# Performance work log

Hardware: AMD Instinct MI355X
Metric: run time of the kernel (lower is better)

## Reference

```python
import jax, jax.numpy as jnp
import numpy as np
from jax.ops import segment_sum

N, E, F, H, G, T = 50000, 800000, 128, 256, 512, 4


def setup_inputs() -> dict:
    key = jax.random.key(0)
    ks = jax.random.split(key, 12)
    x = jax.random.normal(ks[0], (N, F), jnp.float32)
    edge_index = jax.random.randint(ks[1], (2, E), 0, N)
    batch = jnp.sort(jax.random.randint(ks[2], (N,), 0, G))
    num_atoms = jax.random.normal(ks[3], (G, 1), jnp.float32)
    def lin(k, fan_in, fan_out):
        s = 1.0 / np.sqrt(fan_in)
        return jax.random.uniform(k, (fan_in, fan_out), jnp.float32, -s, s)
    W1 = lin(ks[4], F, H); b1 = jnp.zeros((H,), jnp.float32)
    W2 = lin(ks[5], H, H); b2 = jnp.zeros((H,), jnp.float32)
    W3 = lin(ks[6], H + 1, 32); b3 = jnp.zeros((32,), jnp.float32)
    W4 = lin(ks[7], 32, T); b4 = jnp.zeros((T,), jnp.float32)
    return {"x": x, "edge_index": edge_index, "batch": batch, "num_atoms": num_atoms,
            "W1": W1, "b1": b1, "W2": W2, "b2": b2, "W3": W3, "b3": b3, "W4": W4, "b4": b4}


def _gcn_norm(edge_index, num_nodes):
    # PyG GCNConv default: add self-loops, symmetric D^-1/2 A D^-1/2 normalization
    loop = jnp.arange(num_nodes, dtype=edge_index.dtype)
    src = jnp.concatenate([edge_index[0], loop])
    dst = jnp.concatenate([edge_index[1], loop])
    deg = segment_sum(jnp.ones_like(dst, jnp.float32), dst, num_segments=num_nodes)
    dinv = jnp.where(deg > 0, jax.lax.rsqrt(jnp.maximum(deg, 1e-12)), 0.0)
    norm = dinv[src] * dinv[dst]  # [E+N]
    return src, dst, norm


def _gcn_conv(x, W, b, src, dst, norm, num_nodes):
    h = x @ W  # [N, out]
    agg = segment_sum(h[src] * norm[:, None], dst, num_segments=num_nodes)
    return agg + b


def reference(x, edge_index, batch, num_atoms, W1, b1, W2, b2, W3, b3, W4, b4):
    n = x.shape[0]
    src, dst, norm = _gcn_norm(edge_index, n)
    h = jax.nn.relu(_gcn_conv(x, W1, b1, src, dst, norm, n))   # dropout = identity (eval)
    h = jax.nn.relu(_gcn_conv(h, W2, b2, src, dst, norm, n))
    # global mean pool over graphs
    sums = segment_sum(h, batch, num_segments=G)               # [G, H]
    cnt = segment_sum(jnp.ones((n,), jnp.float32), batch, num_segments=G)
    pooled = sums / jnp.maximum(cnt, 1.0)[:, None]
    z = jnp.concatenate([pooled, num_atoms], axis=1)           # [G, H+1]
    z = jax.nn.relu(z @ W3 + b3)
    return z @ W4 + b4                                         # [G, T]
```

## Files before the change

### kernel.cpp

```cpp
#include <hip/hip_runtime.h>
#include <hip/hip_bf16.h>


#define NN 50000
#define EE 800000
#define FDIM 128
#define HDIM 256
#define GG 512
#define SCAN_NB ((NN + 255) / 256)

typedef __attribute__((ext_vector_type(8))) short short8;
typedef __attribute__((ext_vector_type(4))) float floatx4;

__device__ __forceinline__ unsigned short f2bf(float f) {
    unsigned u = __float_as_uint(f);
    return (unsigned short)((u + 0x7FFF + ((u >> 16) & 1)) >> 16);
}
__device__ __forceinline__ float bflo(unsigned v) { return __uint_as_float(v << 16); }
__device__ __forceinline__ float bfhi(unsigned v) { return __uint_as_float(v & 0xFFFF0000u); }


__global__ __launch_bounds__(256) void zero_bufs(int* __restrict__ deg, float* __restrict__ pool) {
    int i = blockIdx.x * 256 + threadIdx.x;
    int stride = gridDim.x * 256;
    for (int k = i; k < NN; k += stride) deg[k] = 0;
    for (int k = i; k < GG * HDIM; k += stride) pool[k] = 0.f;
}

__global__ void hist_kernel(const int* __restrict__ dst, int* __restrict__ deg, int e) {
    int i = blockIdx.x * blockDim.x + threadIdx.x;
    int stride = gridDim.x * blockDim.x;
    for (; i < e; i += stride) atomicAdd(&deg[dst[i]], 1);
}

__global__ __launch_bounds__(256) void scan_part(const int* __restrict__ deg,
                                                 int* __restrict__ row_off,
                                                 int* __restrict__ blk_sums,
                                                 float* __restrict__ dinv, int n) {
    __shared__ int s[256];
    int tid = threadIdx.x;
    int i = blockIdx.x * 256 + tid;
    int v = (i < n) ? deg[i] : 0;
    if (i < n) dinv[i] = rsqrtf((float)v + 1.0f);
    s[tid] = v;
    __syncthreads();
    #pragma unroll
    for (int off = 1; off < 256; off <<= 1) {
        int t = (tid >= off) ? s[tid - off] : 0;
        __syncthreads();
        s[tid] += t;
        __syncthreads();
    }
    if (i < n) row_off[i] = s[tid] - v;
    if (tid == 255) blk_sums[blockIdx.x] = s[255];
}

__global__ __launch_bounds__(256) void scan_sums(int* __restrict__ blk_sums, int nb) {
    __shared__ int s[256];
    int tid = threadIdx.x;
    int v = (tid < nb) ? blk_sums[tid] : 0;
    s[tid] = v;
    __syncthreads();
    #pragma unroll
    for (int off = 1; off < 256; off <<= 1) {
        int t = (tid >= off) ? s[tid - off] : 0;
        __syncthreads();
        s[tid] += t;
        __syncthreads();
    }
    if (tid < nb) blk_sums[tid] = s[tid] - v;
}

__global__ __launch_bounds__(256) void scan_add(int* __restrict__ row_off,
                                                const int* __restrict__ blk_sums,
                                                int* __restrict__ fill, int n, int e) {
    int i = blockIdx.x * 256 + threadIdx.x;
    if (i < n) {
        row_off[i] += blk_sums[blockIdx.x];
        fill[i] = 0;
    }
    if (i == 0) row_off[n] = e;
}

__global__ void scatter_kernel(const int* __restrict__ src, const int* __restrict__ dst,
                               const int* __restrict__ row_off, int* __restrict__ fill,
                               const float* __restrict__ dinv,
                               int2* __restrict__ csr, int e) {
    int i = blockIdx.x * blockDim.x + threadIdx.x;
    int stride = gridDim.x * blockDim.x;
    for (; i < e; i += stride) {
        int s = src[i], d = dst[i];
        int pos = row_off[d] + atomicAdd(&fill[d], 1);
        csr[pos] = make_int2(s, __float_as_int(dinv[s] * dinv[d]));
    }
}

#define XCHUNKS (NN * FDIM / 4)
__global__ __launch_bounds__(256) void cast_all(const float* __restrict__ x,
                                                unsigned short* __restrict__ x_bf,
                                                const float* __restrict__ W1,
                                                unsigned short* __restrict__ W1t,
                                                const float* __restrict__ W2,
                                                unsigned short* __restrict__ W2t) {
    int idx = blockIdx.x * 256 + threadIdx.x;
    if (idx < XCHUNKS) {
        int i = idx * 4;
        float4 v = *(const float4*)&x[i];
        ushort4 o;
        o.x = f2bf(v.x); o.y = f2bf(v.y); o.z = f2bf(v.z); o.w = f2bf(v.w);
        *(ushort4*)&x_bf[i] = o;
        return;
    }
    int r = idx - XCHUNKS;
    if (r < FDIM * HDIM) {
        int nn = r / FDIM, k = r - nn * FDIM;
        W1t[r] = f2bf(W1[(size_t)k * HDIM + nn]);
        return;
    }
    r -= FDIM * HDIM;
    if (r < HDIM * HDIM) {
        int nn = r / HDIM, k = r - nn * HDIM;
        W2t[r] = f2bf(W2[(size_t)k * HDIM + nn]);
    }
}


#define FMA8(v, wgt) do { unsigned _u; \
    _u = (unsigned)(v).x; acc0 = fmaf(bflo(_u), (wgt), acc0); acc1 = fmaf(bfhi(_u), (wgt), acc1); \
    _u = (unsigned)(v).y; acc2 = fmaf(bflo(_u), (wgt), acc2); acc3 = fmaf(bfhi(_u), (wgt), acc3); \
    _u = (unsigned)(v).z; acc4 = fmaf(bflo(_u), (wgt), acc4); acc5 = fmaf(bfhi(_u), (wgt), acc5); \
    _u = (unsigned)(v).w; acc6 = fmaf(bflo(_u), (wgt), acc6); acc7 = fmaf(bfhi(_u), (wgt), acc7); } while (0)

__global__ __launch_bounds__(256) void gcn_agg256_bf16(const unsigned short* __restrict__ in,
                                                       const int* __restrict__ row_off,
                                                       const int2* __restrict__ csr,
                                                       const float* __restrict__ dinv,
                                                       unsigned short* __restrict__ out, int n) {
    int wave = threadIdx.x >> 6;
    int lane = threadIdx.x & 63;
    int node = blockIdx.x * 4 + wave;
    if (node >= n) return;
    int sub = lane >> 5;
    int fl  = lane & 31;
    float di = dinv[node];
    float w0 = (sub == 0) ? di * di : 0.f;

    float acc0, acc1, acc2, acc3, acc4, acc5, acc6, acc7;
    {
        int4 sv = *(const int4*)&in[(size_t)node * 256 + fl * 8];
        unsigned _u;
        _u = (unsigned)sv.x; acc0 = bflo(_u) * w0; acc1 = bfhi(_u) * w0;
        _u = (unsigned)sv.y; acc2 = bflo(_u) * w0; acc3 = bfhi(_u) * w0;
        _u = (unsigned)sv.z; acc4 = bflo(_u) * w0; acc5 = bfhi(_u) * w0;
        _u = (unsigned)sv.w; acc6 = bflo(_u) * w0; acc7 = bfhi(_u) * w0;
    }

    int beg = __builtin_amdgcn_readfirstlane(row_off[node]);
    int end = __builtin_amdgcn_readfirstlane(row_off[node + 1]);
    int cnt = end - beg;
    if (cnt > 0) {
        int nIter = (cnt + 7) >> 3;
        int base = beg;
        int last = end - 1;
        int i0 = base + 0 + sub, i1 = base + 2 + sub, i2 = base + 4 + sub, i3 = base + 6 + sub;
        int2 c0 = csr[i0 < end ? i0 : last];
        int2 c1 = csr[i1 < end ? i1 : last];
        int2 c2 = csr[i2 < end ? i2 : last];
        int2 c3 = csr[i3 < end ? i3 : last];
        for (int it = 0; it < nIter; ++it) {
            int4 g0 = *(const int4*)&in[(size_t)c0.x * 256 + fl * 8];
            int4 g1 = *(const int4*)&in[(size_t)c1.x * 256 + fl * 8];
            int4 g2 = *(const int4*)&in[(size_t)c2.x * 256 + fl * 8];
            int4 g3 = *(const int4*)&in[(size_t)c3.x * 256 + fl * 8];
            float we0 = (base + 0 + sub < end) ? __int_as_float(c0.y) : 0.f;
            float we1 = (base + 2 + sub < end) ? __int_as_float(c1.y) : 0.f;
            float we2 = (base + 4 + sub < end) ? __int_as_float(c2.y) : 0.f;
            float we3 = (base + 6 + sub < end) ? __int_as_float(c3.y) : 0.f;
            int nb = base + 8;
            int j0 = nb + 0 + sub, j1 = nb + 2 + sub, j2 = nb + 4 + sub, j3 = nb + 6 + sub;
            int2 n0 = csr[j0 < end ? j0 : last];
            int2 n1 = csr[j1 < end ? j1 : last];
            int2 n2 = csr[j2 < end ? j2 : last];
            int2 n3 = csr[j3 < end ? j3 : last];
            FMA8(g0, we0); FMA8(g1, we1); FMA8(g2, we2); FMA8(g3, we3);
            c0 = n0; c1 = n1; c2 = n2; c3 = n3; base = nb;
        }
    }
    acc0 += __shfl_xor(acc0, 32); acc1 += __shfl_xor(acc1, 32);
    acc2 += __shfl_xor(acc2, 32); acc3 += __shfl_xor(acc3, 32);
    acc4 += __shfl_xor(acc4, 32); acc5 += __shfl_xor(acc5, 32);
    acc6 += __shfl_xor(acc6, 32); acc7 += __shfl_xor(acc7, 32);
    if (sub == 0) {
        int4 o;
        o.x = (int)((unsigned)f2bf(acc0) | ((unsigned)f2bf(acc1) << 16));
        o.y = (int)((unsigned)f2bf(acc2) | ((unsigned)f2bf(acc3) << 16));
        o.z = (int)((unsigned)f2bf(acc4) | ((unsigned)f2bf(acc5) << 16));
        o.w = (int)((unsigned)f2bf(acc6) | ((unsigned)f2bf(acc7) << 16));
        *(int4*)&out[(size_t)node * 256 + fl * 8] = o;
    }
}

__global__ __launch_bounds__(256) void gcn_agg128_bf16(const unsigned short* __restrict__ in,
                                                       const int* __restrict__ row_off,
                                                       const int2* __restrict__ csr,
                                                       const float* __restrict__ dinv,
                                                       unsigned short* __restrict__ out, int n) {
    int wave = threadIdx.x >> 6;
    int lane = threadIdx.x & 63;
    int node = blockIdx.x * 4 + wave;
    if (node >= n) return;
    int sub = lane >> 4;
    int fl  = lane & 15;
    float di = dinv[node];
    float w0 = (sub == 0) ? di * di : 0.f;

    float acc0, acc1, acc2, acc3, acc4, acc5, acc6, acc7;
    {
        int4 sv = *(const int4*)&in[(size_t)node * 128 + fl * 8];
        unsigned _u;
        _u = (unsigned)sv.x; acc0 = bflo(_u) * w0; acc1 = bfhi(_u) * w0;
        _u = (unsigned)sv.y; acc2 = bflo(_u) * w0; acc3 = bfhi(_u) * w0;
        _u = (unsigned)sv.z; acc4 = bflo(_u) * w0; acc5 = bfhi(_u) * w0;
        _u = (unsigned)sv.w; acc6 = bflo(_u) * w0; acc7 = bfhi(_u) * w0;
    }

    int beg = __builtin_amdgcn_readfirstlane(row_off[node]);
    int end = __builtin_amdgcn_readfirstlane(row_off[node + 1]);
    int cnt = end - beg;
    if (cnt > 0) {
        int nIter = (cnt + 7) >> 3;
        int base = beg;
        int last = end - 1;
        int i0 = base + sub, i1 = base + 4 + sub;
        int2 c0 = csr[i0 < end ? i0 : last];
        int2 c1 = csr[i1 < end ? i1 : last];
        for (int it = 0; it < nIter; ++it) {
            int4 g0 = *(const int4*)&in[(size_t)c0.x * 128 + fl * 8];
            int4 g1 = *(const int4*)&in[(size_t)c1.x * 128 + fl * 8];
            float we0 = (base + sub < end) ? __int_as_float(c0.y) : 0.f;
            float we1 = (base + 4 + sub < end) ? __int_as_float(c1.y) : 0.f;
            int nb = base + 8;
            int j0 = nb + sub, j1 = nb + 4 + sub;
            int2 n0 = csr[j0 < end ? j0 : last];
            int2 n1 = csr[j1 < end ? j1 : last];
            FMA8(g0, we0); FMA8(g1, we1);
            c0 = n0; c1 = n1; base = nb;
        }
    }
    acc0 += __shfl_xor(acc0, 16); acc1 += __shfl_xor(acc1, 16);
    acc2 += __shfl_xor(acc2, 16); acc3 += __shfl_xor(acc3, 16);
    acc4 += __shfl_xor(acc4, 16); acc5 += __shfl_xor(acc5, 16);
    acc6 += __shfl_xor(acc6, 16); acc7 += __shfl_xor(acc7, 16);
    acc0 += __shfl_xor(acc0, 32); acc1 += __shfl_xor(acc1, 32);
    acc2 += __shfl_xor(acc2, 32); acc3 += __shfl_xor(acc3, 32);
    acc4 += __shfl_xor(acc4, 32); acc5 += __shfl_xor(acc5, 32);
    acc6 += __shfl_xor(acc6, 32); acc7 += __shfl_xor(acc7, 32);
    if (sub == 0) {
        int4 o;
        o.x = (int)((unsigned)f2bf(acc0) | ((unsigned)f2bf(acc1) << 16));
        o.y = (int)((unsigned)f2bf(acc2) | ((unsigned)f2bf(acc3) << 16));
        o.z = (int)((unsigned)f2bf(acc4) | ((unsigned)f2bf(acc5) << 16));
        o.w = (int)((unsigned)f2bf(acc6) | ((unsigned)f2bf(acc7) << 16));
        *(int4*)&out[(size_t)node * 128 + fl * 8] = o;
    }
}


__global__ __launch_bounds__(512, 2) void gemm1_mfma_bias_relu(
        const unsigned short* __restrict__ A,
        const unsigned short* __restrict__ Bt,
        const float* __restrict__ bias,
        unsigned short* __restrict__ C, int M) {
    constexpr int K = FDIM, Nc = HDIM, LDT = 40;
    __shared__ unsigned short As[128 * LDT];
    __shared__ unsigned short Bs[256 * LDT];
    int tid = threadIdx.x;
    int lane = tid & 63, wave = tid >> 6;
    int wm = (wave >> 2) * 64, wn = (wave & 3) * 64;
    int bm = blockIdx.x * 128;
    int l15 = lane & 15, quad = lane >> 4;

    floatx4 zero = {0.f, 0.f, 0.f, 0.f};
    floatx4 acc[4][4];
    #pragma unroll
    for (int s = 0; s < 4; ++s)
        #pragma unroll
        for (int t = 0; t < 4; ++t) acc[s][t] = zero;

    for (int k0 = 0; k0 < K; k0 += 32) {
        {
            int row = tid >> 2, q = tid & 3;
            int4 va = {0, 0, 0, 0};
            int gr = bm + row;
            if (gr < M) va = *(const int4*)&A[(size_t)gr * K + k0 + q * 8];
            *(int4*)&As[row * LDT + q * 8] = va;
        }
        #pragma unroll
        for (int c = tid; c < 1024; c += 512) {
            int row = c >> 2, q = c & 3;
            int4 vb = *(const int4*)&Bt[(size_t)row * K + k0 + q * 8];
            *(int4*)&Bs[row * LDT + q * 8] = vb;
        }
        __syncthreads();
        short8 af[4], bf[4];
        #pragma unroll
        for (int s = 0; s < 4; ++s)
            af[s] = *(const short8*)&As[(wm + s * 16 + l15) * LDT + quad * 8];
        #pragma unroll
        for (int t = 0; t < 4; ++t)
            bf[t] = *(const short8*)&Bs[(wn + t * 16 + l15) * LDT + quad * 8];
        #pragma unroll
        for (int s = 0; s < 4; ++s)
            #pragma unroll
            for (int t = 0; t < 4; ++t)
                acc[s][t] = __builtin_amdgcn_mfma_f32_16x16x32_bf16(af[s], bf[t], acc[s][t], 0, 0, 0);
        __syncthreads();
    }
    #pragma unroll
    for (int s = 0; s < 4; ++s) {
        int row0 = bm + wm + s * 16 + quad * 4;
        #pragma unroll
        for (int t = 0; t < 4; ++t) {
            int col = wn + t * 16 + l15;
            float bb = bias[col];
            #pragma unroll
            for (int r = 0; r < 4; ++r) {
                int row = row0 + r;
                if (row < M)
                    C[(size_t)row * Nc + col] = f2bf(fmaxf(acc[s][t][r] + bb, 0.f));
            }
        }
    }
}

__global__ __launch_bounds__(512, 2) void gemm2_pool(
        const unsigned short* __restrict__ A,
        const unsigned short* __restrict__ Bt,
        const float* __restrict__ bias,
        const int* __restrict__ batch,
        float* __restrict__ pool, int M) {
    constexpr int K = HDIM, Nc = HDIM, LDT = 40;
    __shared__ unsigned short As[128 * LDT];
    __shared__ unsigned short Bs[256 * LDT];
    int tid = threadIdx.x;
    int lane = tid & 63, wave = tid >> 6;
    int wm = (wave >> 2) * 64, wn = (wave & 3) * 64;
    int bm = blockIdx.x * 128;
    int l15 = lane & 15, quad = lane >> 4;

    floatx4 zero = {0.f, 0.f, 0.f, 0.f};
    floatx4 acc[4][4];
    #pragma unroll
    for (int s = 0; s < 4; ++s)
        #pragma unroll
        for (int t = 0; t < 4; ++t) acc[s][t] = zero;

    for (int k0 = 0; k0 < K; k0 += 32) {
        {
            int row = tid >> 2, q = tid & 3;
            int4 va = {0, 0, 0, 0};
            int gr = bm + row;
            if (gr < M) va = *(const int4*)&A[(size_t)gr * K + k0 + q * 8];
            *(int4*)&As[row * LDT + q * 8] = va;
        }
        #pragma unroll
        for (int c = tid; c < 1024; c += 512) {
            int row = c >> 2, q = c & 3;
            int4 vb = *(const int4*)&Bt[(size_t)row * K + k0 + q * 8];
            *(int4*)&Bs[row * LDT + q * 8] = vb;
        }
        __syncthreads();
        short8 af[4], bf[4];
        #pragma unroll
        for (int s = 0; s < 4; ++s)
            af[s] = *(const short8*)&As[(wm + s * 16 + l15) * LDT + quad * 8];
        #pragma unroll
        for (int t = 0; t < 4; ++t)
            bf[t] = *(const short8*)&Bs[(wn + t * 16 + l15) * LDT + quad * 8];
        #pragma unroll
        for (int s = 0; s < 4; ++s)
            #pragma unroll
            for (int t = 0; t < 4; ++t)
                acc[s][t] = __builtin_amdgcn_mfma_f32_16x16x32_bf16(af[s], bf[t], acc[s][t], 0, 0, 0);
        __syncthreads();
    }
    #pragma unroll
    for (int s = 0; s < 4; ++s) {
        int row0 = bm + wm + s * 16 + quad * 4;
        if (row0 >= M) continue;
        bool full = (row0 + 3 < M);
        int gA = batch[row0];
        int gB = full ? batch[row0 + 3] : gA;
        bool same = full && (gA == gB);
        #pragma unroll
        for (int t = 0; t < 4; ++t) {
            int col = wn + t * 16 + l15;
            float bb = bias[col];
            if (same) {
                float v = fmaxf(acc[s][t][0] + bb, 0.f) + fmaxf(acc[s][t][1] + bb, 0.f)
                        + fmaxf(acc[s][t][2] + bb, 0.f) + fmaxf(acc[s][t][3] + bb, 0.f);
                atomicAdd(&pool[(size_t)gA * Nc + col], v);
            } else {
                #pragma unroll
                for (int r = 0; r < 4; ++r) {
                    int row = row0 + r;
                    if (row < M) {
                        float v = fmaxf(acc[s][t][r] + bb, 0.f);
                        atomicAdd(&pool[(size_t)batch[row] * Nc + col], v);
                    }
                }
            }
        }
    }
}


__device__ __forceinline__ int lower_bound_i(const int* __restrict__ a, int n, int v) {
    int lo = 0, hi = n;
    while (lo < hi) {
        int mid = (lo + hi) >> 1;
        if (a[mid] < v) lo = mid + 1; else hi = mid;
    }
    return lo;
}

__global__ __launch_bounds__(256) void head_kernel(const float* __restrict__ pool,
                                                   const int* __restrict__ batch,
                                                   const float* __restrict__ num_atoms,
                                                   const float* __restrict__ W3, const float* __restrict__ b3,
                                                   const float* __restrict__ W4, const float* __restrict__ b4,
                                                   float* __restrict__ out, int n) {
    int g = blockIdx.x;
    int tid = threadIdx.x;
    __shared__ int s_lo, s_hi;
    if (tid == 0) {
        s_lo = lower_bound_i(batch, n, g);
        s_hi = lower_bound_i(batch, n, g + 1);
    }
    __syncthreads();
    float cnt = (float)(s_hi - s_lo);

    __shared__ float zin[HDIM + 1];
    __shared__ float z[32];
    zin[tid] = pool[(size_t)g * HDIM + tid] / fmaxf(cnt, 1.0f);
    if (tid == 0) zin[HDIM] = num_atoms[g];
    __syncthreads();
    if (tid < 32) {
        float a = b3[tid];
        for (int k = 0; k < HDIM + 1; ++k) a = fmaf(zin[k], W3[k * 32 + tid], a);
        z[tid] = fmaxf(a, 0.f);
    }
    __syncthreads();
    if (tid < 4) {
        float a = b4[tid];
        #pragma unroll
        for (int k = 0; k < 32; ++k) a = fmaf(z[k], W4[k * 4 + tid], a);
        out[g * 4 + tid] = a;
    }
}


extern "C" void kernel_launch(void* const* d_in, const int* in_sizes, int n_in,
                              void* d_out, int out_size, void* d_ws, size_t ws_size,
                              hipStream_t stream) {
    const float* x         = (const float*)d_in[0];
    const int*   edge_idx  = (const int*)d_in[1];
    const int*   batch     = (const int*)d_in[2];
    const float* num_atoms = (const float*)d_in[3];
    const float* W1 = (const float*)d_in[4];
    const float* b1 = (const float*)d_in[5];
    const float* W2 = (const float*)d_in[6];
    const float* b2 = (const float*)d_in[7];
    const float* W3 = (const float*)d_in[8];
    const float* b3 = (const float*)d_in[9];
    const float* W4 = (const float*)d_in[10];
    const float* b4 = (const float*)d_in[11];
    float* out = (float*)d_out;

    const int n = NN, e = EE;
    const int* e_src = edge_idx;
    const int* e_dst = edge_idx + e;

    char* ws = (char*)d_ws;
    size_t off = 0;
    auto carve = [&](size_t bytes) -> void* {
        void* p = ws + off;
        off = (off + bytes + 255) & ~(size_t)255;
        return p;
    };
    int*   deg_i    = (int*)carve((size_t)n * 4);
    int*   row_off  = (int*)carve((size_t)(n + 1) * 4);
    int*   fill     = (int*)carve((size_t)n * 4);
    int*   blk_sums = (int*)carve((size_t)256 * 4);
    float* dinv     = (float*)carve((size_t)n * 4);
    unsigned short* W1t = (unsigned short*)carve((size_t)FDIM * HDIM * 2);
    unsigned short* W2t = (unsigned short*)carve((size_t)HDIM * HDIM * 2);
    int2*  csr      = (int2*)carve((size_t)e * 8);
    unsigned short* P = (unsigned short*)carve((size_t)n * HDIM * 2);
    unsigned short* Q = (unsigned short*)carve((size_t)n * HDIM * 2);
    float* pool     = (float*)carve((size_t)GG * HDIM * 4);
    unsigned short* x_bf = P;
    unsigned short* a0b  = P + (size_t)n * FDIM;
    unsigned short* a1b  = P;
    unsigned short* h1b  = Q;
    (void)ws_size; (void)n_in; (void)in_sizes; (void)out_size;

    zero_bufs<<<256, 256, 0, stream>>>(deg_i, pool);
    hist_kernel<<<1024, 256, 0, stream>>>(e_dst, deg_i, e);
    scan_part<<<SCAN_NB, 256, 0, stream>>>(deg_i, row_off, blk_sums, dinv, n);
    scan_sums<<<1, 256, 0, stream>>>(blk_sums, SCAN_NB);
    scan_add<<<SCAN_NB, 256, 0, stream>>>(row_off, blk_sums, fill, n, e);
    scatter_kernel<<<1024, 256, 0, stream>>>(e_src, e_dst, row_off, fill, dinv, csr, e);

    cast_all<<<(XCHUNKS + FDIM * HDIM + HDIM * HDIM + 255) / 256, 256, 0, stream>>>(
        x, x_bf, W1, W1t, W2, W2t);

    int gemm_grid = (n + 127) / 128;
    gcn_agg128_bf16<<<(n + 3) / 4, 256, 0, stream>>>(x_bf, row_off, csr, dinv, a0b, n);
    gemm1_mfma_bias_relu<<<gemm_grid, 512, 0, stream>>>(a0b, W1t, b1, h1b, n);
    gcn_agg256_bf16<<<(n + 3) / 4, 256, 0, stream>>>(h1b, row_off, csr, dinv, a1b, n);
    gemm2_pool<<<gemm_grid, 512, 0, stream>>>(a1b, W2t, b2, batch, pool, n);
    head_kernel<<<GG, 256, 0, stream>>>(pool, batch, num_atoms, W3, b3, W4, b4, out, n);
}
```

Baseline: 350.2 us.

## Fuse GCN neighbor aggregation into MFMA GEMM via shared-memory tile

Merges each aggregation kernel with the following GEMM. A block aggregates 32 nodes into an LDS tile, then runs MFMA against the weight matrix read straight from global memory. This drops the intermediate aggregated-activation buffers and two kernel launches. In exchange, GEMM tiles become smaller (32 rows), B fragments are re-read from global/L2 by every block, and each wave handles 8 nodes serially, which may reduce latency hiding in the gather.

```diff
diff --git a/kernel.cpp b/kernel.cpp
--- a/kernel.cpp
+++ b/kernel.cpp
@@ -131,194 +131,105 @@
     _u = (unsigned)(v).z; acc4 = fmaf(bflo(_u), (wgt), acc4); acc5 = fmaf(bfhi(_u), (wgt), acc5); \
     _u = (unsigned)(v).w; acc6 = fmaf(bflo(_u), (wgt), acc6); acc7 = fmaf(bfhi(_u), (wgt), acc7); } while (0)
 
-__global__ __launch_bounds__(256) void gcn_agg256_bf16(const unsigned short* __restrict__ in,
-                                                       const int* __restrict__ row_off,
-                                                       const int2* __restrict__ csr,
-                                                       const float* __restrict__ dinv,
-                                                       unsigned short* __restrict__ out, int n) {
-    int wave = threadIdx.x >> 6;
-    int lane = threadIdx.x & 63;
-    int node = blockIdx.x * 4 + wave;
-    if (node >= n) return;
-    int sub = lane >> 5;
-    int fl  = lane & 31;
-    float di = dinv[node];
-    float w0 = (sub == 0) ? di * di : 0.f;
-
-    float acc0, acc1, acc2, acc3, acc4, acc5, acc6, acc7;
-    {
-        int4 sv = *(const int4*)&in[(size_t)node * 256 + fl * 8];
-        unsigned _u;
-        _u = (unsigned)sv.x; acc0 = bflo(_u) * w0; acc1 = bfhi(_u) * w0;
-        _u = (unsigned)sv.y; acc2 = bflo(_u) * w0; acc3 = bfhi(_u) * w0;
-        _u = (unsigned)sv.z; acc4 = bflo(_u) * w0; acc5 = bfhi(_u) * w0;
-        _u = (unsigned)sv.w; acc6 = bflo(_u) * w0; acc7 = bfhi(_u) * w0;
-    }
-
-    int beg = __builtin_amdgcn_readfirstlane(row_off[node]);
-    int end = __builtin_amdgcn_readfirstlane(row_off[node + 1]);
-    int cnt = end - beg;
-    if (cnt > 0) {
-        int nIter = (cnt + 7) >> 3;
-        int base = beg;
-        int last = end - 1;
-        int i0 = base + 0 + sub, i1 = base + 2 + sub, i2 = base + 4 + sub, i3 = base + 6 + sub;
-        int2 c0 = csr[i0 < end ? i0 : last];
-        int2 c1 = csr[i1 < end ? i1 : last];
-        int2 c2 = csr[i2 < end ? i2 : last];
-        int2 c3 = csr[i3 < end ? i3 : last];
-        for (int it = 0; it < nIter; ++it) {
-            int4 g0 = *(const int4*)&in[(size_t)c0.x * 256 + fl * 8];
-            int4 g1 = *(const int4*)&in[(size_t)c1.x * 256 + fl * 8];
-            int4 g2 = *(const int4*)&in[(size_t)c2.x * 256 + fl * 8];
-            int4 g3 = *(const int4*)&in[(size_t)c3.x * 256 + fl * 8];
-            float we0 = (base + 0 + sub < end) ? __int_as_float(c0.y) : 0.f;
-            float we1 = (base + 2 + sub < end) ? __int_as_float(c1.y) : 0.f;
-            float we2 = (base + 4 + sub < end) ? __int_as_float(c2.y) : 0.f;
-            float we3 = (base + 6 + sub < end) ? __int_as_float(c3.y) : 0.f;
-            int nb = base + 8;
-            int j0 = nb + 0 + sub, j1 = nb + 2 + sub, j2 = nb + 4 + sub, j3 = nb + 6 + sub;
-            int2 n0 = csr[j0 < end ? j0 : last];
-            int2 n1 = csr[j1 < end ? j1 : last];
-            int2 n2 = csr[j2 < end ? j2 : last];
-            int2 n3 = csr[j3 < end ? j3 : last];
-            FMA8(g0, we0); FMA8(g1, we1); FMA8(g2, we2); FMA8(g3, we3);
-            c0 = n0; c1 = n1; c2 = n2; c3 = n3; base = nb;
-        }
-    }
-    acc0 += __shfl_xor(acc0, 32); acc1 += __shfl_xor(acc1, 32);
-    acc2 += __shfl_xor(acc2, 32); acc3 += __shfl_xor(acc3, 32);
-    acc4 += __shfl_xor(acc4, 32); acc5 += __shfl_xor(acc5, 32);
-    acc6 += __shfl_xor(acc6, 32); acc7 += __shfl_xor(acc7, 32);
-    if (sub == 0) {
-        int4 o;
-        o.x = (int)((unsigned)f2bf(acc0) | ((unsigned)f2bf(acc1) << 16));
-        o.y = (int)((unsigned)f2bf(acc2) | ((unsigned)f2bf(acc3) << 16));
-        o.z = (int)((unsigned)f2bf(acc4) | ((unsigned)f2bf(acc5) << 16));
-        o.w = (int)((unsigned)f2bf(acc6) | ((unsigned)f2bf(acc7) << 16));
-        *(int4*)&out[(size_t)node * 256 + fl * 8] = o;
-    }
-}
-
-__global__ __launch_bounds__(256) void gcn_agg128_bf16(const unsigned short* __restrict__ in,
-                                                       const int* __restrict__ row_off,
-                                                       const int2* __restrict__ csr,
-                                                       const float* __restrict__ dinv,
-                                                       unsigned short* __restrict__ out, int n) {
-    int wave = threadIdx.x >> 6;
-    int lane = threadIdx.x & 63;
-    int node = blockIdx.x * 4 + wave;
-    if (node >= n) return;
-    int sub = lane >> 4;
-    int fl  = lane & 15;
-    float di = dinv[node];
-    float w0 = (sub == 0) ? di * di : 0.f;
-
-    float acc0, acc1, acc2, acc3, acc4, acc5, acc6, acc7;
-    {
-        int4 sv = *(const int4*)&in[(size_t)node * 128 + fl * 8];
-        unsigned _u;
-        _u = (unsigned)sv.x; acc0 = bflo(_u) * w0; acc1 = bfhi(_u) * w0;
-        _u = (unsigned)sv.y; acc2 = bflo(_u) * w0; acc3 = bfhi(_u) * w0;
-        _u = (unsigned)sv.z; acc4 = bflo(_u) * w0; acc5 = bfhi(_u) * w0;
-        _u = (unsigned)sv.w; acc6 = bflo(_u) * w0; acc7 = bfhi(_u) * w0;
-    }
-
-    int beg = __builtin_amdgcn_readfirstlane(row_off[node]);
-    int end = __builtin_amdgcn_readfirstlane(row_off[node + 1]);
-    int cnt = end - beg;
-    if (cnt > 0) {
-        int nIter = (cnt + 7) >> 3;
-        int base = beg;
-        int last = end - 1;
-        int i0 = base + sub, i1 = base + 4 + sub;
-        int2 c0 = csr[i0 < end ? i0 : last];
-        int2 c1 = csr[i1 < end ? i1 : last];
-        for (int it = 0; it < nIter; ++it) {
-            int4 g0 = *(const int4*)&in[(size_t)c0.x * 128 + fl * 8];
-            int4 g1 = *(const int4*)&in[(size_t)c1.x * 128 + fl * 8];
-            float we0 = (base + sub < end) ? __int_as_float(c0.y) : 0.f;
-            float we1 = (base + 4 + sub < end) ? __int_as_float(c1.y) : 0.f;
-            int nb = base + 8;
-            int j0 = nb + sub, j1 = nb + 4 + sub;
-            int2 n0 = csr[j0 < end ? j0 : last];
-            int2 n1 = csr[j1 < end ? j1 : last];
-            FMA8(g0, we0); FMA8(g1, we1);
-            c0 = n0; c1 = n1; base = nb;
-        }
-    }
-    acc0 += __shfl_xor(acc0, 16); acc1 += __shfl_xor(acc1, 16);
-    acc2 += __shfl_xor(acc2, 16); acc3 += __shfl_xor(acc3, 16);
-    acc4 += __shfl_xor(acc4, 16); acc5 += __shfl_xor(acc5, 16);
-    acc6 += __shfl_xor(acc6, 16); acc7 += __shfl_xor(acc7, 16);
-    acc0 += __shfl_xor(acc0, 32); acc1 += __shfl_xor(acc1, 32);
-    acc2 += __shfl_xor(acc2, 32); acc3 += __shfl_xor(acc3, 32);
-    acc4 += __shfl_xor(acc4, 32); acc5 += __shfl_xor(acc5, 32);
-    acc6 += __shfl_xor(acc6, 32); acc7 += __shfl_xor(acc7, 32);
-    if (sub == 0) {
-        int4 o;
-        o.x = (int)((unsigned)f2bf(acc0) | ((unsigned)f2bf(acc1) << 16));
-        o.y = (int)((unsigned)f2bf(acc2) | ((unsigned)f2bf(acc3) << 16));
-        o.z = (int)((unsigned)f2bf(acc4) | ((unsigned)f2bf(acc5) << 16));
-        o.w = (int)((unsigned)f2bf(acc6) | ((unsigned)f2bf(acc7) << 16));
-        *(int4*)&out[(size_t)node * 128 + fl * 8] = o;
-    }
-}
-
-
-__global__ __launch_bounds__(512, 2) void gemm1_mfma_bias_relu(
-        const unsigned short* __restrict__ A,
-        const unsigned short* __restrict__ Bt,
-        const float* __restrict__ bias,
-        unsigned short* __restrict__ C, int M) {
-    constexpr int K = FDIM, Nc = HDIM, LDT = 40;
-    __shared__ unsigned short As[128 * LDT];
-    __shared__ unsigned short Bs[256 * LDT];
+__global__ __launch_bounds__(256) void agg_gemm1(const unsigned short* __restrict__ in,
+                                                 const int* __restrict__ row_off,
+                                                 const int2* __restrict__ csr,
+                                                 const float* __restrict__ dinv,
+                                                 const unsigned short* __restrict__ Bt,
+                                                 const float* __restrict__ bias,
+                                                 unsigned short* __restrict__ C, int M) {
+    constexpr int K = FDIM, Nc = HDIM, LDT = 136;
+    __shared__ unsigned short As[32 * LDT];
     int tid = threadIdx.x;
     int lane = tid & 63, wave = tid >> 6;
-    int wm = (wave >> 2) * 64, wn = (wave & 3) * 64;
-    int bm = blockIdx.x * 128;
+    int bm = blockIdx.x * 32;
+
+    {
+        int sub = lane >> 4;
+        int fl  = lane & 15;
+        for (int r8 = 0; r8 < 8; ++r8) {
+            int nodeRow = wave * 8 + r8;
+            int node = bm + nodeRow;
+            if (node >= M) break;
+            float di = dinv[node];
+            float w0 = (sub == 0) ? di * di : 0.f;
+            float acc0, acc1, acc2, acc3, acc4, acc5, acc6, acc7;
+            {
+                int4 sv = *(const int4*)&in[(size_t)node * 128 + fl * 8];
+                unsigned _u;
+                _u = (unsigned)sv.x; acc0 = bflo(_u) * w0; acc1 = bfhi(_u) * w0;
+                _u = (unsigned)sv.y; acc2 = bflo(_u) * w0; acc3 = bfhi(_u) * w0;
+                _u = (unsigned)sv.z; acc4 = bflo(_u) * w0; acc5 = bfhi(_u) * w0;
+                _u = (unsigned)sv.w; acc6 = bflo(_u) * w0; acc7 = bfhi(_u) * w0;
+            }
+            int beg = __builtin_amdgcn_readfirstlane(row_off[node]);
+            int end = __builtin_amdgcn_readfirstlane(row_off[node + 1]);
+            if (end > beg) {
+                int last = end - 1;
+                int base = beg;
+                int i0 = base + sub, i1 = base + 4 + sub;
+                int2 c0 = csr[i0 < end ? i0 : last];
+                int2 c1 = csr[i1 < end ? i1 : last];
+                int nIter = (end - beg + 7) >> 3;
+                for (int it = 0; it < nIter; ++it) {
+                    int4 g0 = *(const int4*)&in[(size_t)c0.x * 128 + fl * 8];
+                    int4 g1 = *(const int4*)&in[(size_t)c1.x * 128 + fl * 8];
+                    float we0 = (base + sub < end) ? __int_as_float(c0.y) : 0.f;
+                    float we1 = (base + 4 + sub < end) ? __int_as_float(c1.y) : 0.f;
+                    int nb = base + 8;
+                    int j0 = nb + sub, j1 = nb + 4 + sub;
+                    int2 n0 = csr[j0 < end ? j0 : last];
+                    int2 n1 = csr[j1 < end ? j1 : last];
+                    FMA8(g0, we0); FMA8(g1, we1);
+                    c0 = n0; c1 = n1; base = nb;
+                }
+            }
+            acc0 += __shfl_xor(acc0, 16); acc1 += __shfl_xor(acc1, 16);
+            acc2 += __shfl_xor(acc2, 16); acc3 += __shfl_xor(acc3, 16);
+            acc4 += __shfl_xor(acc4, 16); acc5 += __shfl_xor(acc5, 16);
+            acc6 += __shfl_xor(acc6, 16); acc7 += __shfl_xor(acc7, 16);
+            acc0 += __shfl_xor(acc0, 32); acc1 += __shfl_xor(acc1, 32);
+            acc2 += __shfl_xor(acc2, 32); acc3 += __shfl_xor(acc3, 32);
+            acc4 += __shfl_xor(acc4, 32); acc5 += __shfl_xor(acc5, 32);
+            acc6 += __shfl_xor(acc6, 32); acc7 += __shfl_xor(acc7, 32);
+            if (sub == 0) {
+                int4 o;
+                o.x = (int)((unsigned)f2bf(acc0) | ((unsigned)f2bf(acc1) << 16));
+                o.y = (int)((unsigned)f2bf(acc2) | ((unsigned)f2bf(acc3) << 16));
+                o.z = (int)((unsigned)f2bf(acc4) | ((unsigned)f2bf(acc5) << 16));
+                o.w = (int)((unsigned)f2bf(acc6) | ((unsigned)f2bf(acc7) << 16));
+                *(int4*)&As[nodeRow * LDT + fl * 8] = o;
+            }
+        }
+    }
+    __syncthreads();
+
     int l15 = lane & 15, quad = lane >> 4;
-
+    int wn = wave * 64;
     floatx4 zero = {0.f, 0.f, 0.f, 0.f};
-    floatx4 acc[4][4];
-    #pragma unroll
-    for (int s = 0; s < 4; ++s)
+    floatx4 acc[2][4];
+    #pragma unroll
+    for (int s = 0; s < 2; ++s)
         #pragma unroll
         for (int t = 0; t < 4; ++t) acc[s][t] = zero;
-
+    #pragma unroll
     for (int k0 = 0; k0 < K; k0 += 32) {
-        {
-            int row = tid >> 2, q = tid & 3;
-            int4 va = {0, 0, 0, 0};
-            int gr = bm + row;
-            if (gr < M) va = *(const int4*)&A[(size_t)gr * K + k0 + q * 8];
-            *(int4*)&As[row * LDT + q * 8] = va;
-        }
-        #pragma unroll
-        for (int c = tid; c < 1024; c += 512) {
-            int row = c >> 2, q = c & 3;
-            int4 vb = *(const int4*)&Bt[(size_t)row * K + k0 + q * 8];
-            *(int4*)&Bs[row * LDT + q * 8] = vb;
-        }
-        __syncthreads();
-        short8 af[4], bf[4];
-        #pragma unroll
-        for (int s = 0; s < 4; ++s)
-            af[s] = *(const short8*)&As[(wm + s * 16 + l15) * LDT + quad * 8];
+        short8 af[2], bf[4];
+        #pragma unroll
+        for (int s = 0; s < 2; ++s)
+            af[s] = *(const short8*)&As[(s * 16 + l15) * LDT + k0 + quad * 8];
         #pragma unroll
         for (int t = 0; t < 4; ++t)
-            bf[t] = *(const short8*)&Bs[(wn + t * 16 + l15) * LDT + quad * 8];
-        #pragma unroll
-        for (int s = 0; s < 4; ++s)
+            bf[t] = *(const short8*)&Bt[(size_t)(wn + t * 16 + l15) * K + k0 + quad * 8];
+        #pragma unroll
+        for (int s = 0; s < 2; ++s)
             #pragma unroll
             for (int t = 0; t < 4; ++t)
                 acc[s][t] = __builtin_amdgcn_mfma_f32_16x16x32_bf16(af[s], bf[t], acc[s][t], 0, 0, 0);
-        __syncthreads();
-    }
-    #pragma unroll
-    for (int s = 0; s < 4; ++s) {
-        int row0 = bm + wm + s * 16 + quad * 4;
+    }
+    #pragma unroll
+    for (int s = 0; s < 2; ++s) {
+        int row0 = bm + s * 16 + quad * 4;
         #pragma unroll
         for (int t = 0; t < 4; ++t) {
             int col = wn + t * 16 + l15;
@@ -333,60 +244,112 @@
     }
 }
 
-__global__ __launch_bounds__(512, 2) void gemm2_pool(
-        const unsigned short* __restrict__ A,
-        const unsigned short* __restrict__ Bt,
-        const float* __restrict__ bias,
-        const int* __restrict__ batch,
-        float* __restrict__ pool, int M) {
-    constexpr int K = HDIM, Nc = HDIM, LDT = 40;
-    __shared__ unsigned short As[128 * LDT];
-    __shared__ unsigned short Bs[256 * LDT];
+__global__ __launch_bounds__(256) void agg_gemm2_pool(const unsigned short* __restrict__ in,
+                                                      const int* __restrict__ row_off,
+                                                      const int2* __restrict__ csr,
+                                                      const float* __restrict__ dinv,
+                                                      const unsigned short* __restrict__ Bt,
+                                                      const float* __restrict__ bias,
+                                                      const int* __restrict__ batch,
+                                                      float* __restrict__ pool, int M) {
+    constexpr int K = HDIM, Nc = HDIM, LDT = 264;
+    __shared__ unsigned short As[32 * LDT];
     int tid = threadIdx.x;
     int lane = tid & 63, wave = tid >> 6;
-    int wm = (wave >> 2) * 64, wn = (wave & 3) * 64;
-    int bm = blockIdx.x * 128;
+    int bm = blockIdx.x * 32;
+
+    {
+        int sub = lane >> 5;
+        int fl  = lane & 31;
+        for (int r8 = 0; r8 < 8; ++r8) {
+            int nodeRow = wave * 8 + r8;
+            int node = bm + nodeRow;
+            if (node >= M) break;
+            float di = dinv[node];
+            float w0 = (sub == 0) ? di * di : 0.f;
+            float acc0, acc1, acc2, acc3, acc4, acc5, acc6, acc7;
+            {
+                int4 sv = *(const int4*)&in[(size_t)node * 256 + fl * 8];
+                unsigned _u;
+                _u = (unsigned)sv.x; acc0 = bflo(_u) * w0; acc1 = bfhi(_u) * w0;
+                _u = (unsigned)sv.y; acc2 = bflo(_u) * w0; acc3 = bfhi(_u) * w0;
+                _u = (unsigned)sv.z; acc4 = bflo(_u) * w0; acc5 = bfhi(_u) * w0;
+                _u = (unsigned)sv.w; acc6 = bflo(_u) * w0; acc7 = bfhi(_u) * w0;
+            }
+            int beg = __builtin_amdgcn_readfirstlane(row_off[node]);
+            int end = __builtin_amdgcn_readfirstlane(row_off[node + 1]);
+            if (end > beg) {
+                int last = end - 1;
+                int base = beg;
+                int i0 = base + 0 + sub, i1 = base + 2 + sub;
+                int i2 = base + 4 + sub, i3 = base + 6 + sub;
+                int2 c0 = csr[i0 < end ? i0 : last];
+                int2 c1 = csr[i1 < end ? i1 : last];
+                int2 c2 = csr[i2 < end ? i2 : last];
+                int2 c3 = csr[i3 < end ? i3 : last];
+                int nIter = (end - beg + 7) >> 3;
+                for (int it = 0; it < nIter; ++it) {
+                    int4 g0 = *(const int4*)&in[(size_t)c0.x * 256 + fl * 8];
+                    int4 g1 = *(const int4*)&in[(size_t)c1.x * 256 + fl * 8];
+                    int4 g2 = *(const int4*)&in[(size_t)c2.x * 256 + fl * 8];
+                    int4 g3 = *(const int4*)&in[(size_t)c3.x * 256 + fl * 8];
+                    float we0 = (base + 0 + sub < end) ? __int_as_float(c0.y) : 0.f;
+                    float we1 = (base + 2 + sub < end) ? __int_as_float(c1.y) : 0.f;
+                    float we2 = (base + 4 + sub < end) ? __int_as_float(c2.y) : 0.f;
+                    float we3 = (base + 6 + sub < end) ? __int_as_float(c3.y) : 0.f;
+                    int nb = base + 8;
+                    int j0 = nb + 0 + sub, j1 = nb + 2 + sub;
+                    int j2 = nb + 4 + sub, j3 = nb + 6 + sub;
+                    int2 n0 = csr[j0 < end ? j0 : last];
+                    int2 n1 = csr[j1 < end ? j1 : last];
+                    int2 n2 = csr[j2 < end ? j2 : last];
+                    int2 n3 = csr[j3 < end ? j3 : last];
+                    FMA8(g0, we0); FMA8(g1, we1); FMA8(g2, we2); FMA8(g3, we3);
+                    c0 = n0; c1 = n1; c2 = n2; c3 = n3; base = nb;
+                }
+            }
+            acc0 += __shfl_xor(acc0, 32); acc1 += __shfl_xor(acc1, 32);
+            acc2 += __shfl_xor(acc2, 32); acc3 += __shfl_xor(acc3, 32);
+            acc4 += __shfl_xor(acc4, 32); acc5 += __shfl_xor(acc5, 32);
+            acc6 += __shfl_xor(acc6, 32); acc7 += __shfl_xor(acc7, 32);
+            if (sub == 0) {
+                int4 o;
+                o.x = (int)((unsigned)f2bf(acc0) | ((unsigned)f2bf(acc1) << 16));
+                o.y = (int)((unsigned)f2bf(acc2) | ((unsigned)f2bf(acc3) << 16));
+                o.z = (int)((unsigned)f2bf(acc4) | ((unsigned)f2bf(acc5) << 16));
+                o.w = (int)((unsigned)f2bf(acc6) | ((unsigned)f2bf(acc7) << 16));
+                *(int4*)&As[nodeRow * LDT + fl * 8] = o;
+            }
+        }
+    }
+    __syncthreads();
+
     int l15 = lane & 15, quad = lane >> 4;
-
+    int wn = wave * 64;
     floatx4 zero = {0.f, 0.f, 0.f, 0.f};
-    floatx4 acc[4][4];
-    #pragma unroll
-    for (int s = 0; s < 4; ++s)
+    floatx4 acc[2][4];
+    #pragma unroll
+    for (int s = 0; s < 2; ++s)
         #pragma unroll
         for (int t = 0; t < 4; ++t) acc[s][t] = zero;
-
+    #pragma unroll
     for (int k0 = 0; k0 < K; k0 += 32) {
-        {
-            int row = tid >> 2, q = tid & 3;
-            int4 va = {0, 0, 0, 0};
-            int gr = bm + row;
-            if (gr < M) va = *(const int4*)&A[(size_t)gr * K + k0 + q * 8];
-            *(int4*)&As[row * LDT + q * 8] = va;
-        }
-        #pragma unroll
-        for (int c = tid; c < 1024; c += 512) {
-            int row = c >> 2, q = c & 3;
-            int4 vb = *(const int4*)&Bt[(size_t)row * K + k0 + q * 8];
-            *(int4*)&Bs[row * LDT + q * 8] = vb;
-        }
-        __syncthreads();
-        short8 af[4], bf[4];
-        #pragma unroll
-        for (int s = 0; s < 4; ++s)
-            af[s] = *(const short8*)&As[(wm + s * 16 + l15) * LDT + quad * 8];
+        short8 af[2], bf[4];
+        #pragma unroll
+        for (int s = 0; s < 2; ++s)
+            af[s] = *(const short8*)&As[(s * 16 + l15) * LDT + k0 + quad * 8];
         #pragma unroll
         for (int t = 0; t < 4; ++t)
-            bf[t] = *(const short8*)&Bs[(wn + t * 16 + l15) * LDT + quad * 8];
-        #pragma unroll
-        for (int s = 0; s < 4; ++s)
+            bf[t] = *(const short8*)&Bt[(size_t)(wn + t * 16 + l15) * K + k0 + quad * 8];
+        #pragma unroll
+        for (int s = 0; s < 2; ++s)
             #pragma unroll
             for (int t = 0; t < 4; ++t)
                 acc[s][t] = __builtin_amdgcn_mfma_f32_16x16x32_bf16(af[s], bf[t], acc[s][t], 0, 0, 0);
-        __syncthreads();
-    }
-    #pragma unroll
-    for (int s = 0; s < 4; ++s) {
-        int row0 = bm + wm + s * 16 + quad * 4;
+    }
+    #pragma unroll
+    for (int s = 0; s < 2; ++s) {
+        int row0 = bm + s * 16 + quad * 4;
         if (row0 >= M) continue;
         bool full = (row0 + 3 < M);
         int gA = batch[row0];
@@ -496,13 +459,9 @@
     unsigned short* W1t = (unsigned short*)carve((size_t)FDIM * HDIM * 2);
     unsigned short* W2t = (unsigned short*)carve((size_t)HDIM * HDIM * 2);
     int2*  csr      = (int2*)carve((size_t)e * 8);
-    unsigned short* P = (unsigned short*)carve((size_t)n * HDIM * 2);
-    unsigned short* Q = (unsigned short*)carve((size_t)n * HDIM * 2);
+    unsigned short* x_bf = (unsigned short*)carve((size_t)n * FDIM * 2);
+    unsigned short* h1b  = (unsigned short*)carve((size_t)n * HDIM * 2);
     float* pool     = (float*)carve((size_t)GG * HDIM * 4);
-    unsigned short* x_bf = P;
-    unsigned short* a0b  = P + (size_t)n * FDIM;
-    unsigned short* a1b  = P;
-    unsigned short* h1b  = Q;
     (void)ws_size; (void)n_in; (void)in_sizes; (void)out_size;
 
     zero_bufs<<<256, 256, 0, stream>>>(deg_i, pool);
@@ -515,10 +474,8 @@
     cast_all<<<(XCHUNKS + FDIM * HDIM + HDIM * HDIM + 255) / 256, 256, 0, stream>>>(
         x, x_bf, W1, W1t, W2, W2t);
 
-    int gemm_grid = (n + 127) / 128;
-    gcn_agg128_bf16<<<(n + 3) / 4, 256, 0, stream>>>(x_bf, row_off, csr, dinv, a0b, n);
-    gemm1_mfma_bias_relu<<<gemm_grid, 512, 0, stream>>>(a0b, W1t, b1, h1b, n);
-    gcn_agg256_bf16<<<(n + 3) / 4, 256, 0, stream>>>(h1b, row_off, csr, dinv, a1b, n);
-    gemm2_pool<<<gemm_grid, 512, 0, stream>>>(a1b, W2t, b2, batch, pool, n);
+    int fused_grid = (n + 31) / 32;
+    agg_gemm1<<<fused_grid, 256, 0, stream>>>(x_bf, row_off, csr, dinv, W1t, b1, h1b, n);
+    agg_gemm2_pool<<<fused_grid, 256, 0, stream>>>(h1b, row_off, csr, dinv, W2t, b2, batch, pool, n);
     head_kernel<<<GG, 256, 0, stream>>>(pool, batch, num_atoms, W3, b3, W4, b4, out, n);
 }
```

Result: slower. 381.0 us (+8.8%).
